# Optimization experiments

Hardware: AMD Instinct MI355X
Metric: run time of the kernel (lower is better)

Reference implementation:

```python
import jax, jax.numpy as jnp
import numpy as np

B, S, D = 8, 2048, 1024


def setup_inputs() -> dict:
    key = jax.random.key(0)
    ks = jax.random.split(key, 10)
    s = 0.02
    x = jax.random.normal(ks[0], (B, S, D), dtype=jnp.float32)
    # causal boolean mask [B, S, S]
    mask = jnp.broadcast_to(jnp.tril(jnp.ones((S, S), dtype=bool)), (B, S, S))
    Wq = jax.random.normal(ks[1], (D, D), dtype=jnp.float32) * s
    bq = jax.random.normal(ks[2], (D,), dtype=jnp.float32) * s
    Wk = jax.random.normal(ks[3], (D, D), dtype=jnp.float32) * s
    bk = jax.random.normal(ks[4], (D,), dtype=jnp.float32) * s
    Wv = jax.random.normal(ks[5], (D, D), dtype=jnp.float32) * s
    bv = jax.random.normal(ks[6], (D,), dtype=jnp.float32) * s
    Wo = jax.random.normal(ks[7], (D, D), dtype=jnp.float32) * s
    bo = jax.random.normal(ks[8], (D,), dtype=jnp.float32) * s
    return {"x": x, "mask": mask, "Wq": Wq, "bq": bq, "Wk": Wk, "bk": bk,
            "Wv": Wv, "bv": bv, "Wo": Wo, "bo": bo}


def reference(x, mask, Wq, bq, Wk, bk, Wv, bv, Wo, bo):
    # no cache -> cache_len = 0, full x/mask used; dropout=0.0 (identity)
    d_k = x.shape[-1]
    q = jnp.einsum('bsd,ed->bse', x, Wq) + bq
    k = jnp.einsum('bsd,ed->bse', x, Wk) + bk  # computed but unused (original bug)
    v = jnp.einsum('bsd,ed->bse', x, Wv) + bv
    # NOTE: original code uses q @ v^T (not k) - reproduced faithfully
    scores = jnp.einsum('bqd,bkd->bqk', q, v) / jnp.sqrt(jnp.float32(d_k))
    scores = jnp.where(mask, scores, jnp.float32(-jnp.inf))
    attn = jax.nn.softmax(scores, axis=-1)
    ctx = jnp.einsum('bqk,bkd->bqd', attn, v)
    out = jnp.einsum('bsd,ed->bse', ctx, Wo) + bo
    return out
```

## Files before the change

### kernel.cpp

```cpp
#include <hip/hip_runtime.h>

typedef unsigned short u16;
typedef __attribute__((ext_vector_type(8))) unsigned short u16x8;
typedef __bf16 bf16x8 __attribute__((ext_vector_type(8)));
typedef float f32x4 __attribute__((ext_vector_type(4)));

__device__ __forceinline__ u16 f2b(float f) {
    unsigned u = __float_as_uint(f);
    u += 0x7fffu + ((u >> 16) & 1u);
    return (u16)(u >> 16);
}
__device__ __forceinline__ float b2f(u16 h) {
    return __uint_as_float(((unsigned)h) << 16);
}

__device__ __forceinline__ void async_copy16(const void* g, void* l) {
    __builtin_amdgcn_global_load_lds(
        (const __attribute__((address_space(1))) unsigned int*)g,
        (__attribute__((address_space(3))) unsigned int*)l,
        16, 0, 0);
}

__device__ __forceinline__ int swz(int x) { return x ^ (((x >> 7) & 7) << 4); }

__global__ __launch_bounds__(256) void cast_kernel(const float* __restrict__ in,
                                                   u16* __restrict__ out, long n) {
    long i0 = ((long)blockIdx.x * 256 + threadIdx.x) * 8;
    long stride = (long)gridDim.x * 256 * 8;
    for (long i = i0; i < n; i += stride) {
        float4 a = *(const float4*)(in + i);
        float4 b = *(const float4*)(in + i + 4);
        u16x8 o;
        o[0] = f2b(a.x); o[1] = f2b(a.y); o[2] = f2b(a.z); o[3] = f2b(a.w);
        o[4] = f2b(b.x); o[5] = f2b(b.y); o[6] = f2b(b.z); o[7] = f2b(b.w);
        *(u16x8*)(out + i) = o;
    }
}

__global__ __launch_bounds__(256) void cast3_kernel(const float* __restrict__ w0,
                                                    const float* __restrict__ w1,
                                                    const float* __restrict__ w2,
                                                    u16* __restrict__ o0,
                                                    u16* __restrict__ o1,
                                                    u16* __restrict__ o2, long n) {
    int z = blockIdx.z;
    const float* in = (z == 0) ? w0 : (z == 1) ? w1 : w2;
    u16* out = (z == 0) ? o0 : (z == 1) ? o1 : o2;
    long i = ((long)blockIdx.x * 256 + threadIdx.x) * 8;
    if (i < n) {
        float4 a = *(const float4*)(in + i);
        float4 b = *(const float4*)(in + i + 4);
        u16x8 o;
        o[0] = f2b(a.x); o[1] = f2b(a.y); o[2] = f2b(a.z); o[3] = f2b(a.w);
        o[4] = f2b(b.x); o[5] = f2b(b.y); o[6] = f2b(b.z); o[7] = f2b(b.w);
        *(u16x8*)(out + i) = o;
    }
}

__global__ __launch_bounds__(256) void transpose_kernel(const u16* __restrict__ in,
                                                        u16* __restrict__ out,
                                                        int S_, int D_) {
    __shared__ u16 tile[64 * 64];
    long base = (long)blockIdx.z * (long)S_ * D_;
    int r0 = blockIdx.y * 64;
    int c0 = blockIdx.x * 64;
    int t = threadIdx.x;
    {
        int r = t >> 3, cb = (t & 7) * 16;
        #pragma unroll
        for (int h = 0; h < 2; ++h) {
            int rr = r + h * 32;
            u16x8 d8 = *(const u16x8*)(in + base + (long)(r0 + rr) * D_ + c0 + (cb >> 1));
            int phys = rr * 128 + (cb ^ (((rr >> 3) & 7) << 4));
            *(u16x8*)((char*)tile + phys) = d8;
        }
    }
    __syncthreads();
    {
        int od = t & 63;
        int gb = (t >> 6) * 2;
        #pragma unroll
        for (int h = 0; h < 2; ++h) {
            int g = gb + h;
            u16x8 o8;
            #pragma unroll
            for (int j = 0; j < 8; ++j) {
                int rr = g * 8 + j;
                int phys = rr * 128 + ((od * 2) ^ (((rr >> 3) & 7) << 4));
                o8[j] = *(const u16*)((char*)tile + phys);
            }
            *(u16x8*)(out + base + (long)(c0 + od) * S_ + r0 + g * 8) = o8;
        }
    }
}

__global__ __launch_bounds__(256) void softmax_kernel(u16* __restrict__ Sc) {
    const int SS = 2048;
    long row = blockIdx.x;
    int q = (int)(row & (SS - 1));
    int L = q + 1;
    int Klim = ((q >> 8) + 1) << 8;
    u16* p = Sc + row * SS;
    int tid = threadIdx.x;
    int i0 = tid * 8;

    float v[8];
    if (i0 < Klim) {
        u16x8 raw = *(const u16x8*)(p + i0);
        #pragma unroll
        for (int j = 0; j < 8; ++j)
            v[j] = (i0 + j < L) ? b2f(raw[j]) : -1e30f;
    } else {
        #pragma unroll
        for (int j = 0; j < 8; ++j) v[j] = -1e30f;
    }

    float m = v[0];
    #pragma unroll
    for (int j = 1; j < 8; ++j) m = fmaxf(m, v[j]);
    #pragma unroll
    for (int o = 32; o > 0; o >>= 1) m = fmaxf(m, __shfl_xor(m, o));
    __shared__ float red[8];
    if ((tid & 63) == 0) red[tid >> 6] = m;
    __syncthreads();
    m = fmaxf(fmaxf(red[0], red[1]), fmaxf(red[2], red[3]));

    float e[8];
    float s = 0.f;
    #pragma unroll
    for (int j = 0; j < 8; ++j) { e[j] = __expf(v[j] - m); s += e[j]; }
    #pragma unroll
    for (int o = 32; o > 0; o >>= 1) s += __shfl_xor(s, o);
    if ((tid & 63) == 0) red[4 + (tid >> 6)] = s;
    __syncthreads();
    s = red[4] + red[5] + red[6] + red[7];
    float inv = 1.f / s;

    if (i0 < Klim) {
        u16x8 o8;
        #pragma unroll
        for (int j = 0; j < 8; ++j) o8[j] = f2b(e[j] * inv);
        *(u16x8*)(p + i0) = o8;
    }
}

template<typename OUTT, bool BIAS, bool CSKIP, bool KLIM>
__global__ __launch_bounds__(512)
void gemm256(const u16* __restrict__ Aall, const u16* __restrict__ Ball,
             const float* __restrict__ bias, const float* __restrict__ bias2,
             OUTT* __restrict__ Call,
             int M, int N, int K, float scale, long sA, long sB, long sC) {
    const int bz = blockIdx.z;
    const u16* A = Aall + (long)bz * sA;
    const u16* B = Ball + (long)bz * sB;
    OUTT* C = Call + (long)bz * sC;
    const float* bp = (bz && bias2) ? bias2 : bias;
    const int bm = blockIdx.y, bn = blockIdx.x;
    if (CSKIP && bn > bm) return;
    int Keff = K;
    if (KLIM) { int kl = (bm + 1) * 256; Keff = kl < K ? kl : K; }
    const int NT = Keff >> 6;

    extern __shared__ __align__(16) char lds[];

    const int tid = threadIdx.x;
    const int lane = tid & 63;
    const int w = tid >> 6;
    const int wm = w >> 2, wn = w & 3;
    const int fr = lane & 15, hi = lane >> 4;
    const int axor = (fr & 7) << 4;

    const long rowA0 = (long)bm * 256;
    const long rowB0 = (long)bn * 256;

    auto stage_half = [&](const u16* mat, long gr0, int k0, char* region) {
        #pragma unroll
        for (int rd = 0; rd < 2; ++rd) {
            int pb = rd * 8192 + w * 1024;
            int p = pb + lane * 16;
            int Lb = swz(p);
            const u16* src = mat + (gr0 + (Lb >> 7)) * (long)K + k0 + ((Lb & 127) >> 1);
            async_copy16(src, region + pb);
        }
    };

    f32x4 acc[8][4] = {};
    bf16x8 a[4][2], b0[2][2], b1[2][2];

    char* bufp0 = lds;
    char* bufp1 = lds + 65536;

    stage_half(A, rowA0,       0, bufp0 + 0 * 16384);
    stage_half(B, rowB0,       0, bufp0 + 2 * 16384);
    stage_half(B, rowB0 + 128, 0, bufp0 + 3 * 16384);
    stage_half(A, rowA0 + 128, 0, bufp0 + 1 * 16384);
    asm volatile("s_waitcnt vmcnt(4)" ::: "memory");
    if (1 < NT) {
        stage_half(A, rowA0,       64, bufp1 + 0 * 16384);
        stage_half(B, rowB0,       64, bufp1 + 2 * 16384);
        stage_half(B, rowB0 + 128, 64, bufp1 + 3 * 16384);
    }
    asm volatile("s_waitcnt vmcnt(6)" ::: "memory");
    __builtin_amdgcn_s_barrier();

    const int abase = (wm * 64 + fr) * 128 + hi * 16;
    const int bbase = (wn * 32 + fr) * 128 + hi * 16;

    for (int u = 0; u < NT; ++u) {
        char* bufp  = (u & 1) ? bufp1 : bufp0;
        char* obufp = (u & 1) ? bufp0 : bufp1;

        #pragma unroll
        for (int m = 0; m < 4; ++m)
            #pragma unroll
            for (int kk = 0; kk < 2; ++kk)
                a[m][kk] = *(const bf16x8*)(bufp + 0 * 16384 + ((abase + m * 2048 + kk * 64) ^ axor));
        #pragma unroll
        for (int nl = 0; nl < 2; ++nl)
            #pragma unroll
            for (int kk = 0; kk < 2; ++kk)
                b0[nl][kk] = *(const bf16x8*)(bufp + 2 * 16384 + ((bbase + nl * 2048 + kk * 64) ^ axor));
        if (u + 1 < NT)
            stage_half(A, rowA0 + 128, (u + 1) * 64, obufp + 1 * 16384);
        asm volatile("s_waitcnt lgkmcnt(8)" ::: "memory");
        __builtin_amdgcn_s_barrier();
        asm volatile("s_waitcnt lgkmcnt(0)" ::: "memory");
        __builtin_amdgcn_sched_barrier(0);
        __builtin_amdgcn_s_setprio(1);
        #pragma unroll
        for (int m = 0; m < 4; ++m)
            #pragma unroll
            for (int nl = 0; nl < 2; ++nl)
                #pragma unroll
                for (int kk = 0; kk < 2; ++kk)
                    acc[m][nl] = __builtin_amdgcn_mfma_f32_16x16x32_bf16(a[m][kk], b0[nl][kk], acc[m][nl], 0, 0, 0);
        __builtin_amdgcn_s_setprio(0);
        __builtin_amdgcn_s_barrier();

        #pragma unroll
        for (int nl = 0; nl < 2; ++nl)
            #pragma unroll
            for (int kk = 0; kk < 2; ++kk)
                b1[nl][kk] = *(const bf16x8*)(bufp + 3 * 16384 + ((bbase + nl * 2048 + kk * 64) ^ axor));
        if (u + 2 < NT)
            stage_half(A, rowA0, (u + 2) * 64, bufp + 0 * 16384);
        __builtin_amdgcn_s_barrier();
        asm volatile("s_waitcnt lgkmcnt(0)" ::: "memory");
        __builtin_amdgcn_sched_barrier(0);
        __builtin_amdgcn_s_setprio(1);
        #pragma unroll
        for (int m = 0; m < 4; ++m)
            #pragma unroll
            for (int nl = 0; nl < 2; ++nl)
                #pragma unroll
                for (int kk = 0; kk < 2; ++kk)
                    acc[m][2 + nl] = __builtin_amdgcn_mfma_f32_16x16x32_bf16(a[m][kk], b1[nl][kk], acc[m][2 + nl], 0, 0, 0);
        __builtin_amdgcn_s_setprio(0);
        __builtin_amdgcn_s_barrier();

        #pragma unroll
        for (int m = 0; m < 4; ++m)
            #pragma unroll
            for (int kk = 0; kk < 2; ++kk)
                a[m][kk] = *(const bf16x8*)(bufp + 1 * 16384 + ((abase + m * 2048 + kk * 64) ^ axor));
        if (u + 2 < NT)
            stage_half(B, rowB0, (u + 2) * 64, bufp + 2 * 16384);
        __builtin_amdgcn_s_barrier();
        asm volatile("s_waitcnt lgkmcnt(0)" ::: "memory");
        __builtin_amdgcn_sched_barrier(0);
        __builtin_amdgcn_s_setprio(1);
        #pragma unroll
        for (int m = 0; m < 4; ++m)
            #pragma unroll
            for (int nl = 0; nl < 2; ++nl)
                #pragma unroll
                for (int kk = 0; kk < 2; ++kk)
                    acc[4 + m][2 + nl] = __builtin_amdgcn_mfma_f32_16x16x32_bf16(a[m][kk], b1[nl][kk], acc[4 + m][2 + nl], 0, 0, 0);
        __builtin_amdgcn_s_setprio(0);
        __builtin_amdgcn_s_barrier();

        if (u + 2 < NT)
            stage_half(B, rowB0 + 128, (u + 2) * 64, bufp + 3 * 16384);
        __builtin_amdgcn_s_barrier();
        __builtin_amdgcn_s_setprio(1);
        #pragma unroll
        for (int m = 0; m < 4; ++m)
            #pragma unroll
            for (int nl = 0; nl < 2; ++nl)
                #pragma unroll
                for (int kk = 0; kk < 2; ++kk)
                    acc[4 + m][nl] = __builtin_amdgcn_mfma_f32_16x16x32_bf16(a[m][kk], b0[nl][kk], acc[4 + m][nl], 0, 0, 0);
        __builtin_amdgcn_s_setprio(0);
        if (u < NT - 2) { asm volatile("s_waitcnt vmcnt(6)" ::: "memory"); }
        else            { asm volatile("s_waitcnt vmcnt(0)" ::: "memory"); }
        __builtin_amdgcn_s_barrier();
    }

    #pragma unroll
    for (int m = 0; m < 8; ++m) {
        int rl = (m < 4) ? (wm * 64 + m * 16) : (128 + wm * 64 + (m - 4) * 16);
        long grow = rowA0 + rl + hi * 4;
        #pragma unroll
        for (int n = 0; n < 4; ++n) {
            int cl = (n < 2) ? (wn * 32 + n * 16) : (128 + wn * 32 + (n - 2) * 16);
            long gcol = rowB0 + cl + fr;
            float bvv = BIAS ? bp[gcol] : 0.f;
            #pragma unroll
            for (int j = 0; j < 4; ++j) {
                float v = acc[m][n][j] * scale + bvv;
                if constexpr (sizeof(OUTT) == 2) {
                    C[(grow + j) * N + gcol] = (OUTT)f2b(v);
                } else {
                    C[(grow + j) * N + gcol] = v;
                }
            }
        }
    }
}

template<int MODE>
__global__ __launch_bounds__(512)
void gemm128(const u16* __restrict__ Aall, const u16* __restrict__ Ball,
             u16* __restrict__ Call, int N, int K, float scale,
             long sA, long sB, long sC) {
    extern __shared__ __align__(16) char lds[];
    const int tid = threadIdx.x;
    const int lane = tid & 63;
    const int w = tid >> 6;
    const int wm = w >> 2, wn = w & 3;
    const int fr = lane & 15, hi = lane >> 4;
    const int axor = (fr & 7) << 4;
    const int abase = (wm * 64 + fr) * 128 + hi * 16;
    const int bbase = (wn * 32 + fr) * 128 + hi * 16;

    auto run_tile = [&](const u16* A, const u16* B, u16* C,
                        long rowA0, long colB0, int Keff) {
        const int NT = Keff >> 6;
        auto stage = [&](const u16* mat, long gr0, int k0, char* region) {
            #pragma unroll
            for (int rd = 0; rd < 2; ++rd) {
                int pb = rd * 8192 + w * 1024;
                int p = pb + lane * 16;
                int Lb = swz(p);
                const u16* src = mat + (gr0 + (Lb >> 7)) * (long)K + k0 + ((Lb & 127) >> 1);
                async_copy16(src, region + pb);
            }
        };
        char* bf0 = lds;
        char* bf1 = lds + 49152;
        f32x4 acc[8][2] = {};
        bf16x8 a[4][2], bb[2][2];

        stage(A, rowA0,       0, bf0 + 0);
        stage(B, colB0,       0, bf0 + 32768);
        stage(A, rowA0 + 128, 0, bf0 + 16384);
        if (1 < NT) {
            stage(A, rowA0, 64, bf1 + 0);
            stage(B, colB0, 64, bf1 + 32768);
        }
        asm volatile("s_waitcnt vmcnt(6)" ::: "memory");
        __builtin_amdgcn_s_barrier();

        for (int u = 0; u < NT; ++u) {
            char* cb = (u & 1) ? bf1 : bf0;
            char* ob = (u & 1) ? bf0 : bf1;

            #pragma unroll
            for (int m = 0; m < 4; ++m)
                #pragma unroll
                for (int kk = 0; kk < 2; ++kk)
                    a[m][kk] = *(const bf16x8*)(cb + ((abase + m * 2048 + kk * 64) ^ axor));
            #pragma unroll
            for (int nl = 0; nl < 2; ++nl)
                #pragma unroll
                for (int kk = 0; kk < 2; ++kk)
                    bb[nl][kk] = *(const bf16x8*)(cb + 32768 + ((bbase + nl * 2048 + kk * 64) ^ axor));
            if (u + 1 < NT)
                stage(A, rowA0 + 128, (u + 1) * 64, ob + 16384);
            asm volatile("s_waitcnt lgkmcnt(8)" ::: "memory");
            __builtin_amdgcn_s_barrier();
            asm volatile("s_waitcnt lgkmcnt(0)" ::: "memory");
            __builtin_amdgcn_sched_barrier(0);
            __builtin_amdgcn_s_setprio(1);
            #pragma unroll
            for (int m = 0; m < 4; ++m)
                #pragma unroll
                for (int nl = 0; nl < 2; ++nl)
                    #pragma unroll
                    for (int kk = 0; kk < 2; ++kk)
                        acc[m][nl] = __builtin_amdgcn_mfma_f32_16x16x32_bf16(a[m][kk], bb[nl][kk], acc[m][nl], 0, 0, 0);
            __builtin_amdgcn_s_setprio(0);
            if (u < NT - 1) { asm volatile("s_waitcnt vmcnt(6)" ::: "memory"); }
            else            { asm volatile("s_waitcnt vmcnt(0)" ::: "memory"); }
            __builtin_amdgcn_s_barrier();

            #pragma unroll
            for (int m = 0; m < 4; ++m)
                #pragma unroll
                for (int kk = 0; kk < 2; ++kk)
                    a[m][kk] = *(const bf16x8*)(cb + 16384 + ((abase + m * 2048 + kk * 64) ^ axor));
            if (u + 2 < NT) {
                stage(A, rowA0, (u + 2) * 64, cb + 0);
                stage(B, colB0, (u + 2) * 64, cb + 32768);
            }
            __builtin_amdgcn_s_barrier();
            asm volatile("s_waitcnt lgkmcnt(0)" ::: "memory");
            __builtin_amdgcn_sched_barrier(0);
            __builtin_amdgcn_s_setprio(1);
            #pragma unroll
            for (int m = 0; m < 4; ++m)
                #pragma unroll
                for (int nl = 0; nl < 2; ++nl)
                    #pragma unroll
                    for (int kk = 0; kk < 2; ++kk)
                        acc[4 + m][nl] = __builtin_amdgcn_mfma_f32_16x16x32_bf16(a[m][kk], bb[nl][kk], acc[4 + m][nl], 0, 0, 0);
            __builtin_amdgcn_s_setprio(0);
            if (u < NT - 2)      { asm volatile("s_waitcnt vmcnt(6)" ::: "memory"); }
            else if (u == NT - 2){ asm volatile("s_waitcnt vmcnt(2)" ::: "memory"); }
            else                 { asm volatile("s_waitcnt vmcnt(0)" ::: "memory"); }
            __builtin_amdgcn_s_barrier();
        }

        #pragma unroll
        for (int m = 0; m < 8; ++m) {
            int rl = (m < 4) ? (wm * 64 + m * 16) : (128 + wm * 64 + (m - 4) * 16);
            long grow = rowA0 + rl + hi * 4;
            #pragma unroll
            for (int n = 0; n < 2; ++n) {
                long gcol = colB0 + wn * 32 + n * 16 + fr;
                #pragma unroll
                for (int j = 0; j < 4; ++j)
                    C[(grow + j) * N + gcol] = f2b(acc[m][n][j] * scale);
            }
        }
    };

    if constexpr (MODE == 0) {
        int bn = blockIdx.x, pp = blockIdx.y, bz = blockIdx.z;
        const u16* A = Aall + (long)bz * sA;
        const u16* B = Ball + (long)bz * sB;
        u16* C = Call + (long)bz * sC;
        #pragma unroll
        for (int r = 0; r < 2; ++r) {
            int bm = r ? (7 - pp) : pp;
            run_tile(A, B, C, (long)bm * 256, (long)bn * 128, (bm + 1) * 256);
        }
    } else {
        for (int f = blockIdx.x; f < 576; f += 256) {
            int b = f / 72, t = f - b * 72;
            int bm = 0;
            #pragma unroll
            for (int r = 1; r < 8; ++r) bm = (t >= r * r + r) ? r : bm;
            int bn = t - (bm * bm + bm);
            run_tile(Aall + (long)b * sA, Ball + (long)b * sB, Call + (long)b * sC,
                     (long)bm * 256, (long)bn * 128, K);
        }
    }
}

extern "C" void kernel_launch(void* const* d_in, const int* in_sizes, int n_in,
                              void* d_out, int out_size, void* d_ws, size_t ws_size,
                              hipStream_t stream) {
    (void)in_sizes; (void)n_in; (void)out_size; (void)ws_size;
    const float* x  = (const float*)d_in[0];
    const float* Wq = (const float*)d_in[2];
    const float* bq = (const float*)d_in[3];
    const float* Wv = (const float*)d_in[6];
    const float* bv = (const float*)d_in[7];
    const float* Wo = (const float*)d_in[8];
    const float* bo = (const float*)d_in[9];
    float* out = (float*)d_out;

    const long B = 8, S = 2048, D = 1024;
    const long MS = B * S;

    char* p = (char*)d_ws;
    u16* xb  = (u16*)p; p += MS * D * 2;
    u16* Wqb = (u16*)p; p += D * D * 2;
    u16* Wvb = (u16*)p; p += D * D * 2;
    u16* Wob = (u16*)p; p += D * D * 2;
    u16* Qb  = (u16*)p; p += MS * D * 2;
    u16* Vb  = (u16*)p; p += MS * D * 2;
    u16* Sb  = (u16*)p; p += B * S * S * 2;
    u16* ctxb = xb;
    u16* Vtb  = Qb;

    const int SMEM256 = 131072, SMEM128 = 98304;
    (void)hipFuncSetAttribute((const void*)gemm256<u16, true, false, false>,
                              hipFuncAttributeMaxDynamicSharedMemorySize, SMEM256);
    (void)hipFuncSetAttribute((const void*)gemm256<float, true, false, false>,
                              hipFuncAttributeMaxDynamicSharedMemorySize, SMEM256);
    (void)hipFuncSetAttribute((const void*)gemm128<0>,
                              hipFuncAttributeMaxDynamicSharedMemorySize, SMEM128);
    (void)hipFuncSetAttribute((const void*)gemm128<1>,
                              hipFuncAttributeMaxDynamicSharedMemorySize, SMEM128);

    cast_kernel<<<4096, 256, 0, stream>>>(x, xb, MS * D);
    cast3_kernel<<<dim3(512, 1, 3), 256, 0, stream>>>(Wq, Wv, Wo, Wqb, Wvb, Wob, D * D);

    dim3 gqv(D / 256, MS / 256, 2);
    gemm256<u16, true, false, false><<<gqv, 512, SMEM256, stream>>>(
        xb, Wqb, bq, bv, Qb, (int)MS, (int)D, (int)D, 1.0f, 0, D * D, MS * D);

    gemm128<1><<<dim3(256, 1, 1), 512, SMEM128, stream>>>(
        Qb, Vb, Sb, (int)S, (int)D, 0.03125f, S * D, S * D, S * S);

    softmax_kernel<<<MS, 256, 0, stream>>>(Sb);

    dim3 gtr(D / 64, S / 64, B);
    transpose_kernel<<<gtr, 256, 0, stream>>>(Vb, Vtb, (int)S, (int)D);

    gemm128<0><<<dim3(8, 4, 8), 512, SMEM128, stream>>>(
        Sb, Vtb, ctxb, (int)D, (int)S, 1.0f, S * S, D * S, S * D);

    dim3 gproj(D / 256, MS / 256, 1);
    gemm256<float, true, false, false><<<gproj, 512, SMEM256, stream>>>(
        ctxb, Wob, bo, nullptr, out, (int)MS, (int)D, (int)D, 1.0f, 0, 0, 0);
}
```

Before: 516.8 us.

## Fuse softmax into score and context GEMMs via unnormalized exp and rowsum atomics

Removes the standalone softmax kernel. The score GEMM now writes the masked exp of the scaled scores (no max subtraction) and atomically adds per-row sums into a zeroed buffer. The context GEMM divides its output rows by those sums. Grids are flattened to 1D with an XCD-aware block mapping so blocks sharing operands land on the same XCD. Skipping max subtraction risks overflow if scores grow large, and the atomics add contention.

```diff
diff --git a/kernel.cpp b/kernel.cpp
--- a/kernel.cpp
+++ b/kernel.cpp
@@ -57,6 +57,11 @@
     }
 }
 
+__global__ __launch_bounds__(256) void zero_kernel(float* __restrict__ p, long n4) {
+    long i = (long)blockIdx.x * 256 + threadIdx.x;
+    if (i < n4) ((float4*)p)[i] = float4{0.f, 0.f, 0.f, 0.f};
+}
+
 __global__ __launch_bounds__(256) void transpose_kernel(const u16* __restrict__ in,
                                                         u16* __restrict__ out,
                                                         int S_, int D_) {
@@ -94,72 +99,26 @@
     }
 }
 
-__global__ __launch_bounds__(256) void softmax_kernel(u16* __restrict__ Sc) {
-    const int SS = 2048;
-    long row = blockIdx.x;
-    int q = (int)(row & (SS - 1));
-    int L = q + 1;
-    int Klim = ((q >> 8) + 1) << 8;
-    u16* p = Sc + row * SS;
-    int tid = threadIdx.x;
-    int i0 = tid * 8;
-
-    float v[8];
-    if (i0 < Klim) {
-        u16x8 raw = *(const u16x8*)(p + i0);
-        #pragma unroll
-        for (int j = 0; j < 8; ++j)
-            v[j] = (i0 + j < L) ? b2f(raw[j]) : -1e30f;
+template<int MODE, typename OUTT>
+__global__ __launch_bounds__(512)
+void gemm_u(const u16* __restrict__ Aall, const u16* __restrict__ Ball,
+            const float* __restrict__ bias, const float* __restrict__ bias2,
+            OUTT* __restrict__ Call,
+            int N, int K, long sB, long sC) {
+    const int id = blockIdx.x;
+    int bm, bn, z = 0;
+    if constexpr (MODE == 0) {
+        int xcd = id & 7, s = id >> 3;
+        z = s >> 5; bm = xcd + 8 * ((s >> 2) & 7); bn = s & 3;
     } else {
-        #pragma unroll
-        for (int j = 0; j < 8; ++j) v[j] = -1e30f;
-    }
-
-    float m = v[0];
-    #pragma unroll
-    for (int j = 1; j < 8; ++j) m = fmaxf(m, v[j]);
-    #pragma unroll
-    for (int o = 32; o > 0; o >>= 1) m = fmaxf(m, __shfl_xor(m, o));
-    __shared__ float red[8];
-    if ((tid & 63) == 0) red[tid >> 6] = m;
-    __syncthreads();
-    m = fmaxf(fmaxf(red[0], red[1]), fmaxf(red[2], red[3]));
-
-    float e[8];
-    float s = 0.f;
-    #pragma unroll
-    for (int j = 0; j < 8; ++j) { e[j] = __expf(v[j] - m); s += e[j]; }
-    #pragma unroll
-    for (int o = 32; o > 0; o >>= 1) s += __shfl_xor(s, o);
-    if ((tid & 63) == 0) red[4 + (tid >> 6)] = s;
-    __syncthreads();
-    s = red[4] + red[5] + red[6] + red[7];
-    float inv = 1.f / s;
-
-    if (i0 < Klim) {
-        u16x8 o8;
-        #pragma unroll
-        for (int j = 0; j < 8; ++j) o8[j] = f2b(e[j] * inv);
-        *(u16x8*)(p + i0) = o8;
-    }
-}
-
-template<typename OUTT, bool BIAS, bool CSKIP, bool KLIM>
-__global__ __launch_bounds__(512)
-void gemm256(const u16* __restrict__ Aall, const u16* __restrict__ Ball,
-             const float* __restrict__ bias, const float* __restrict__ bias2,
-             OUTT* __restrict__ Call,
-             int M, int N, int K, float scale, long sA, long sB, long sC) {
-    const int bz = blockIdx.z;
-    const u16* A = Aall + (long)bz * sA;
-    const u16* B = Ball + (long)bz * sB;
-    OUTT* C = Call + (long)bz * sC;
-    const float* bp = (bz && bias2) ? bias2 : bias;
-    const int bm = blockIdx.y, bn = blockIdx.x;
-    if (CSKIP && bn > bm) return;
-    int Keff = K;
-    if (KLIM) { int kl = (bm + 1) * 256; Keff = kl < K ? kl : K; }
-    const int NT = Keff >> 6;
+        int xcd = id & 7, s = id >> 3;
+        bm = xcd + 8 * (s >> 2); bn = s & 3;
+    }
+    const u16* A = Aall;
+    const u16* B = Ball + (long)z * sB;
+    OUTT* C = Call + (long)z * sC;
+    const float* bp = z ? bias2 : bias;
+    const int NT = K >> 6;
 
     extern __shared__ __align__(16) char lds[];
 
@@ -304,10 +263,10 @@
         for (int n = 0; n < 4; ++n) {
             int cl = (n < 2) ? (wn * 32 + n * 16) : (128 + wn * 32 + (n - 2) * 16);
             long gcol = rowB0 + cl + fr;
-            float bvv = BIAS ? bp[gcol] : 0.f;
+            float bvv = bp[gcol];
             #pragma unroll
             for (int j = 0; j < 4; ++j) {
-                float v = acc[m][n][j] * scale + bvv;
+                float v = acc[m][n][j] + bvv;
                 if constexpr (sizeof(OUTT) == 2) {
                     C[(grow + j) * N + gcol] = (OUTT)f2b(v);
                 } else {
@@ -320,9 +279,9 @@
 
 template<int MODE>
 __global__ __launch_bounds__(512)
-void gemm128(const u16* __restrict__ Aall, const u16* __restrict__ Ball,
-             u16* __restrict__ Call, int N, int K, float scale,
-             long sA, long sB, long sC) {
+void gemm_h(const u16* __restrict__ Aall, const u16* __restrict__ Ball,
+            u16* __restrict__ Call, float* __restrict__ rowsum,
+            int N, int K, float scale, long sA, long sB, long sC) {
     extern __shared__ __align__(16) char lds[];
     const int tid = threadIdx.x;
     const int lane = tid & 63;
@@ -333,15 +292,19 @@
     const int abase = (wm * 64 + fr) * 128 + hi * 16;
     const int bbase = (wn * 32 + fr) * 128 + hi * 16;
 
-    auto run_tile = [&](const u16* A, const u16* B, u16* C,
-                        long rowA0, long colB0, int Keff) {
-        const int NT = Keff >> 6;
+    const int bz = blockIdx.x & 7;
+    const u16* A = Aall + (long)bz * sA;
+    const u16* B = Ball + (long)bz * sB;
+    u16* C = Call + (long)bz * sC;
+    float* rsv = rowsum + bz * 2048;
+
+    auto run_tile = [&](long rowA0, long colB0, int NT, bool domask) {
         auto stage = [&](const u16* mat, long gr0, int k0, char* region) {
             #pragma unroll
             for (int rd = 0; rd < 2; ++rd) {
                 int pb = rd * 8192 + w * 1024;
-                int p = pb + lane * 16;
-                int Lb = swz(p);
+                int pp = pb + lane * 16;
+                int Lb = swz(pp);
                 const u16* src = mat + (gr0 + (Lb >> 7)) * (long)K + k0 + ((Lb & 127) >> 1);
                 async_copy16(src, region + pb);
             }
@@ -415,9 +378,8 @@
                     for (int kk = 0; kk < 2; ++kk)
                         acc[4 + m][nl] = __builtin_amdgcn_mfma_f32_16x16x32_bf16(a[m][kk], bb[nl][kk], acc[4 + m][nl], 0, 0, 0);
             __builtin_amdgcn_s_setprio(0);
-            if (u < NT - 2)      { asm volatile("s_waitcnt vmcnt(6)" ::: "memory"); }
-            else if (u == NT - 2){ asm volatile("s_waitcnt vmcnt(2)" ::: "memory"); }
-            else                 { asm volatile("s_waitcnt vmcnt(0)" ::: "memory"); }
+            if (u < NT - 2) { asm volatile("s_waitcnt vmcnt(6)" ::: "memory"); }
+            else            { asm volatile("s_waitcnt vmcnt(0)" ::: "memory"); }
             __builtin_amdgcn_s_barrier();
         }
 
@@ -425,35 +387,57 @@
         for (int m = 0; m < 8; ++m) {
             int rl = (m < 4) ? (wm * 64 + m * 16) : (128 + wm * 64 + (m - 4) * 16);
             long grow = rowA0 + rl + hi * 4;
-            #pragma unroll
-            for (int n = 0; n < 2; ++n) {
-                long gcol = colB0 + wn * 32 + n * 16 + fr;
-                #pragma unroll
-                for (int j = 0; j < 4; ++j)
-                    C[(grow + j) * N + gcol] = f2b(acc[m][n][j] * scale);
+            if constexpr (MODE == 2) {
+                float rs_acc[4] = {0.f, 0.f, 0.f, 0.f};
+                #pragma unroll
+                for (int n = 0; n < 2; ++n) {
+                    long gcol = colB0 + wn * 32 + n * 16 + fr;
+                    #pragma unroll
+                    for (int j = 0; j < 4; ++j) {
+                        long r = grow + j;
+                        float e = (!domask || gcol <= r) ? __expf(acc[m][n][j] * scale) : 0.f;
+                        u16 wv = f2b(e);
+                        C[r * N + gcol] = wv;
+                        rs_acc[j] += b2f(wv);
+                    }
+                }
+                #pragma unroll
+                for (int j = 0; j < 4; ++j) {
+                    float v = rs_acc[j];
+                    v += __shfl_xor(v, 1); v += __shfl_xor(v, 2);
+                    v += __shfl_xor(v, 4); v += __shfl_xor(v, 8);
+                    if (fr == 0) atomicAdd(&rsv[(int)(grow + j)], v);
+                }
+            } else {
+                float inv[4];
+                #pragma unroll
+                for (int j = 0; j < 4; ++j) inv[j] = 1.0f / rsv[(int)(grow + j)];
+                #pragma unroll
+                for (int n = 0; n < 2; ++n) {
+                    long gcol = colB0 + wn * 32 + n * 16 + fr;
+                    #pragma unroll
+                    for (int j = 0; j < 4; ++j)
+                        C[(grow + j) * N + gcol] = f2b(acc[m][n][j] * inv[j]);
+                }
             }
         }
     };
 
-    if constexpr (MODE == 0) {
-        int bn = blockIdx.x, pp = blockIdx.y, bz = blockIdx.z;
-        const u16* A = Aall + (long)bz * sA;
-        const u16* B = Ball + (long)bz * sB;
-        u16* C = Call + (long)bz * sC;
+    if constexpr (MODE == 2) {
+        int t = blockIdx.x >> 3;
+        int bm = 0;
+        #pragma unroll
+        for (int c = 1; c < 8; ++c)
+            if (t >= c * c + c) bm = c;
+        int h = t - (bm * bm + bm);
+        run_tile((long)bm * 256, (long)h * 128, K >> 6, h >= 2 * bm);
+    } else {
+        int s = blockIdx.x >> 3;
+        int p = s & 3, bn = s >> 2;
         #pragma unroll
         for (int r = 0; r < 2; ++r) {
-            int bm = r ? (7 - pp) : pp;
-            run_tile(A, B, C, (long)bm * 256, (long)bn * 128, (bm + 1) * 256);
-        }
-    } else {
-        for (int f = blockIdx.x; f < 576; f += 256) {
-            int b = f / 72, t = f - b * 72;
-            int bm = 0;
-            #pragma unroll
-            for (int r = 1; r < 8; ++r) bm = (t >= r * r + r) ? r : bm;
-            int bn = t - (bm * bm + bm);
-            run_tile(Aall + (long)b * sA, Ball + (long)b * sB, Call + (long)b * sC,
-                     (long)bm * 256, (long)bn * 128, K);
+            int bm = r ? (7 - p) : p;
+            run_tile((long)bm * 256, (long)bn * 128, (bm + 1) * 4, false);
         }
     }
 }
@@ -482,38 +466,36 @@
     u16* Qb  = (u16*)p; p += MS * D * 2;
     u16* Vb  = (u16*)p; p += MS * D * 2;
     u16* Sb  = (u16*)p; p += B * S * S * 2;
+    float* rowsum = (float*)p; p += MS * 4;
     u16* ctxb = xb;
     u16* Vtb  = Qb;
 
-    const int SMEM256 = 131072, SMEM128 = 98304;
-    (void)hipFuncSetAttribute((const void*)gemm256<u16, true, false, false>,
-                              hipFuncAttributeMaxDynamicSharedMemorySize, SMEM256);
-    (void)hipFuncSetAttribute((const void*)gemm256<float, true, false, false>,
-                              hipFuncAttributeMaxDynamicSharedMemorySize, SMEM256);
-    (void)hipFuncSetAttribute((const void*)gemm128<0>,
-                              hipFuncAttributeMaxDynamicSharedMemorySize, SMEM128);
-    (void)hipFuncSetAttribute((const void*)gemm128<1>,
-                              hipFuncAttributeMaxDynamicSharedMemorySize, SMEM128);
+    const int SMEM = 131072, SMEMH = 98304;
+    (void)hipFuncSetAttribute((const void*)gemm_u<0, u16>,
+                              hipFuncAttributeMaxDynamicSharedMemorySize, SMEM);
+    (void)hipFuncSetAttribute((const void*)gemm_u<1, float>,
+                              hipFuncAttributeMaxDynamicSharedMemorySize, SMEM);
+    (void)hipFuncSetAttribute((const void*)gemm_h<2>,
+                              hipFuncAttributeMaxDynamicSharedMemorySize, SMEMH);
+    (void)hipFuncSetAttribute((const void*)gemm_h<3>,
+                              hipFuncAttributeMaxDynamicSharedMemorySize, SMEMH);
 
     cast_kernel<<<4096, 256, 0, stream>>>(x, xb, MS * D);
     cast3_kernel<<<dim3(512, 1, 3), 256, 0, stream>>>(Wq, Wv, Wo, Wqb, Wvb, Wob, D * D);
-
-    dim3 gqv(D / 256, MS / 256, 2);
-    gemm256<u16, true, false, false><<<gqv, 512, SMEM256, stream>>>(
-        xb, Wqb, bq, bv, Qb, (int)MS, (int)D, (int)D, 1.0f, 0, D * D, MS * D);
-
-    gemm128<1><<<dim3(256, 1, 1), 512, SMEM128, stream>>>(
-        Qb, Vb, Sb, (int)S, (int)D, 0.03125f, S * D, S * D, S * S);
-
-    softmax_kernel<<<MS, 256, 0, stream>>>(Sb);
+    zero_kernel<<<16, 256, 0, stream>>>(rowsum, MS / 4);
+
+    gemm_u<0, u16><<<512, 512, SMEM, stream>>>(
+        xb, Wqb, bq, bv, Qb, (int)D, (int)D, D * D, MS * D);
+
+    gemm_h<2><<<576, 512, SMEMH, stream>>>(
+        Qb, Vb, Sb, rowsum, (int)S, (int)D, 0.03125f, S * D, S * D, S * S);
 
     dim3 gtr(D / 64, S / 64, B);
     transpose_kernel<<<gtr, 256, 0, stream>>>(Vb, Vtb, (int)S, (int)D);
 
-    gemm128<0><<<dim3(8, 4, 8), 512, SMEM128, stream>>>(
-        Sb, Vtb, ctxb, (int)D, (int)S, 1.0f, S * S, D * S, S * D);
-
-    dim3 gproj(D / 256, MS / 256, 1);
-    gemm256<float, true, false, false><<<gproj, 512, SMEM256, stream>>>(
-        ctxb, Wob, bo, nullptr, out, (int)MS, (int)D, (int)D, 1.0f, 0, 0, 0);
-}
+    gemm_h<3><<<256, 512, SMEMH, stream>>>(
+        Sb, Vtb, ctxb, rowsum, (int)D, (int)S, 1.0f, S * S, D * S, S * D);
+
+    gemm_u<1, float><<<256, 512, SMEM, stream>>>(
+        ctxb, Wob, bo, nullptr, out, (int)D, (int)D, 0, 0);
+}
```

Result: faster. 494.1 us (-4.4%).
